# Kernel tuning notes

Hardware: AMD Instinct MI355X
Metric: run time of the kernel (lower is better)

## Reference

```python
import jax, jax.numpy as jnp
import numpy as np

N_NODES = 50000
N_EDGES = 800000
IN_FEATS = 128
H_FEATS = 128
OUT_FEATS = 64


def _mean_agg(h, src, dst, n_nodes):
    # mean over in-neighbors: sum h[src] into dst, divide by in-degree (0 for isolated nodes)
    summed = jax.ops.segment_sum(h[src], dst, num_segments=n_nodes)  # [N, d]
    deg = jax.ops.segment_sum(jnp.ones((src.shape[0],), h.dtype), dst, num_segments=n_nodes)
    return summed / jnp.maximum(deg, 1.0)[:, None]


def setup_inputs() -> dict:
    key = jax.random.key(0)
    ks = jax.random.split(key, 10)
    s = 0.05
    return {
        "inputs": jax.random.normal(ks[0], (N_NODES, IN_FEATS), jnp.float32),
        "fc_W": jax.random.normal(ks[1], (H_FEATS, IN_FEATS), jnp.float32) * s,
        "fc_b": jax.random.normal(ks[2], (H_FEATS,), jnp.float32) * s,
        "W": jax.random.normal(ks[3], (3, H_FEATS, H_FEATS), jnp.float32) * s,
        "b": jax.random.normal(ks[4], (3, H_FEATS), jnp.float32) * s,
        "W_last": jax.random.normal(ks[5], (OUT_FEATS, H_FEATS), jnp.float32) * s,
        "b_last": jax.random.normal(ks[6], (OUT_FEATS,), jnp.float32) * s,
        "eps": jnp.zeros((4,), jnp.float32),
        "src": jax.random.randint(ks[7], (N_EDGES,), 0, N_NODES, jnp.int32),
        "dst": jax.random.randint(ks[8], (N_EDGES,), 0, N_NODES, jnp.int32),
    }


def reference(inputs, fc_W, fc_b, W, b, W_last, b_last, eps, src, dst):
    n = inputs.shape[0]
    # input SLP
    h = jax.nn.relu(inputs @ fc_W.T + fc_b)
    # 3 hidden GIN layers: relu(Linear((1+eps)*h + mean_agg(h)))  (dropout = eval identity)
    for i in range(3):
        agg = _mean_agg(h, src, dst, n)
        h = jax.nn.relu(((1.0 + eps[i]) * h + agg) @ W[i].T + b[i])
    # last GIN layer (no ReLU)
    agg = _mean_agg(h, src, dst, n)
    h = ((1.0 + eps[3]) * h + agg) @ W_last.T + b_last
    return h
```

## Files before the change

### kernel.cpp

```cpp
#include <hip/hip_runtime.h>

#define N_NODES 50000
#define N_EDGES 800000
#define NBUCK 196
#define CAP 4608
#define CSTRIDE 16
#define EPB 4096
#define NSTRIPE ((N_EDGES + EPB - 1) / EPB)
#define GEMMB 782
#define WSPLB 224

typedef __attribute__((ext_vector_type(8))) short short8;
typedef __attribute__((ext_vector_type(4))) float float4v;

__device__ inline unsigned short f2bf(float f) {
    unsigned u = __float_as_uint(f);
    unsigned r = u + 0x7fff + ((u >> 16) & 1);
    return (unsigned short)(r >> 16);
}
__device__ inline float bf2f(unsigned short h) {
    return __uint_as_float(((unsigned)h) << 16);
}

__device__ __forceinline__ void split8(const float* __restrict__ p, short8& hi8, short8& lo8) {
    float4 f0 = *(const float4*)p;
    float4 f1 = *(const float4*)(p + 4);
    float fv[8] = {f0.x, f0.y, f0.z, f0.w, f1.x, f1.y, f1.z, f1.w};
#pragma unroll
    for (int j = 0; j < 8; j++) {
        unsigned short hh = f2bf(fv[j]);
        hi8[j] = (short)hh;
        lo8[j] = (short)f2bf(fv[j] - bf2f(hh));
    }
}


__device__ __forceinline__ void gather_sum(const unsigned short* __restrict__ bf,
                                           const int* __restrict__ esrc, int beg, int end,
                                           int eg, int fo, float a0[8]) {
    float a1[8], a2[8], a3[8];
#pragma unroll
    for (int j = 0; j < 8; j++) { a0[j] = 0.f; a1[j] = 0.f; a2[j] = 0.f; a3[j] = 0.f; }
    int e = beg;
    for (; e + 15 < end; e += 16) {
        int s0 = esrc[e + eg];
        int s1 = esrc[e + 4 + eg];
        int s2 = esrc[e + 8 + eg];
        int s3 = esrc[e + 12 + eg];
        short8 v0 = *(const short8*)(bf + (size_t)s0 * 128 + fo * 8);
        short8 v1 = *(const short8*)(bf + (size_t)s1 * 128 + fo * 8);
        short8 v2 = *(const short8*)(bf + (size_t)s2 * 128 + fo * 8);
        short8 v3 = *(const short8*)(bf + (size_t)s3 * 128 + fo * 8);
#pragma unroll
        for (int j = 0; j < 8; j++) a0[j] += bf2f((unsigned short)v0[j]);
#pragma unroll
        for (int j = 0; j < 8; j++) a1[j] += bf2f((unsigned short)v1[j]);
#pragma unroll
        for (int j = 0; j < 8; j++) a2[j] += bf2f((unsigned short)v2[j]);
#pragma unroll
        for (int j = 0; j < 8; j++) a3[j] += bf2f((unsigned short)v3[j]);
    }
    if (e + 7 < end) {
        int s0 = esrc[e + eg];
        int s1 = esrc[e + 4 + eg];
        short8 v0 = *(const short8*)(bf + (size_t)s0 * 128 + fo * 8);
        short8 v1 = *(const short8*)(bf + (size_t)s1 * 128 + fo * 8);
#pragma unroll
        for (int j = 0; j < 8; j++) a0[j] += bf2f((unsigned short)v0[j]);
#pragma unroll
        for (int j = 0; j < 8; j++) a1[j] += bf2f((unsigned short)v1[j]);
        e += 8;
    }
    if (e + 3 < end) {
        int s = esrc[e + eg];
        short8 v = *(const short8*)(bf + (size_t)s * 128 + fo * 8);
#pragma unroll
        for (int j = 0; j < 8; j++) a2[j] += bf2f((unsigned short)v[j]);
        e += 4;
    }
    int rem = end - e;
    if (eg < rem) {
        int s = esrc[e + eg];
        short8 v = *(const short8*)(bf + (size_t)s * 128 + fo * 8);
#pragma unroll
        for (int j = 0; j < 8; j++) a3[j] += bf2f((unsigned short)v[j]);
    }
#pragma unroll
    for (int j = 0; j < 8; j++) {
        float s = (a0[j] + a1[j]) + (a2[j] + a3[j]);
        s += __shfl_xor(s, 16);
        s += __shfl_xor(s, 32);
        a0[j] = s;
    }
}


__device__ __forceinline__ void slp_gemm(int bx, const float* __restrict__ X,
                                         const float* __restrict__ fcW,
                                         const float* __restrict__ fcb, float* __restrict__ h,
                                         unsigned short* __restrict__ hbf) {
    int wave = threadIdx.x >> 6;
    int lane = threadIdx.x & 63;
    int m = lane & 15;
    int quad = lane >> 4;
    int r0 = bx * 64 + wave * 16;
    int rowA = r0 + m;
    if (rowA >= N_NODES) rowA = N_NODES - 1;

    short8 ahi[4], alo[4];
    const float* arow = X + (size_t)rowA * 128 + quad * 8;
#pragma unroll
    for (int kc = 0; kc < 4; kc++) split8(arow + kc * 32, ahi[kc], alo[kc]);

#pragma unroll
    for (int nt = 0; nt < 8; nt++) {
        int n = nt * 16 + m;
        const float* brow = fcW + (size_t)n * 128 + quad * 8;
        float4v acc = {0.f, 0.f, 0.f, 0.f};
#pragma unroll
        for (int kc = 0; kc < 4; kc++) {
            short8 bh, bl;
            split8(brow + kc * 32, bh, bl);
            acc = __builtin_amdgcn_mfma_f32_16x16x32_bf16(ahi[kc], bh, acc, 0, 0, 0);
            acc = __builtin_amdgcn_mfma_f32_16x16x32_bf16(alo[kc], bh, acc, 0, 0, 0);
            acc = __builtin_amdgcn_mfma_f32_16x16x32_bf16(ahi[kc], bl, acc, 0, 0, 0);
        }
        float bv = fcb[n];
#pragma unroll
        for (int i = 0; i < 4; i++) {
            int r = r0 + quad * 4 + i;
            if (r < N_NODES) {
                float v = fmaxf(acc[i] + bv, 0.f);
                h[(size_t)r * 128 + n] = v;
                hbf[(size_t)r * 128 + n] = f2bf(v);
            }
        }
    }
}


__global__ void __launch_bounds__(256) fused_binA_gemm(
    const int* __restrict__ src, const int* __restrict__ dst, int* __restrict__ cursor,
    int* __restrict__ packed, const float* __restrict__ X, const float* __restrict__ fcW,
    const float* __restrict__ fcb, const float* __restrict__ W, const float* __restrict__ Wl,
    unsigned short* __restrict__ whi, unsigned short* __restrict__ wlo, float* __restrict__ h,
    unsigned short* __restrict__ hbf) {
    int bx = blockIdx.x;
    if (bx < NSTRIPE) {
        __shared__ int lcount[256];
        __shared__ int lbase[256];
        int t = threadIdx.x;
        lcount[t] = 0;
        __syncthreads();
        int base = bx * EPB + t;
#pragma unroll 4
        for (int k = 0; k < EPB / 256; k++) {
            int i = base + k * 256;
            if (i < N_EDGES) atomicAdd(&lcount[((unsigned)dst[i]) >> 8], 1);
        }
        __syncthreads();
        if (t < NBUCK) {
            lbase[t] = t * CAP + atomicAdd(&cursor[t * CSTRIDE], lcount[t]);
            lcount[t] = 0;
        }
        __syncthreads();
#pragma unroll 4
        for (int k = 0; k < EPB / 256; k++) {
            int i = base + k * 256;
            if (i < N_EDGES) {
                int d = dst[i];
                int wb = ((unsigned)d) >> 8;
                int p = lbase[wb] + atomicAdd(&lcount[wb], 1);
                if (p < (wb + 1) * CAP)
                    packed[p] = ((d & 255) << 16) | src[i];
            }
        }
    } else if (bx < NSTRIPE + GEMMB) {
        slp_gemm(bx - NSTRIPE, X, fcW, fcb, h, hbf);
    } else {
        int i = (bx - NSTRIPE - GEMMB) * 256 + threadIdx.x + 16384;
        if (i < 73728) {
            float v = (i < 65536) ? W[i - 16384] : Wl[i - 65536];
            unsigned short hh = f2bf(v);
            whi[i] = hh;
            wlo[i] = f2bf(v - bf2f(hh));
        }
    }
}


__global__ void __launch_bounds__(256) binB_kernel(const int* __restrict__ packed,
                                                   const int* __restrict__ cursor,
                                                   int* __restrict__ row_ptr,
                                                   int* __restrict__ esrc) {
    __shared__ int sm[256];
    __shared__ int cntS[256];
    __shared__ int curs[256];
    int b = blockIdx.x;
    int t = threadIdx.x;
    int cnt = (t < NBUCK) ? cursor[t * CSTRIDE] : 0;
    cntS[t] = cnt;
    sm[t] = cnt;
    __syncthreads();
    for (int o = 1; o < 256; o <<= 1) {
        int x = sm[t];
        int a = (t >= o) ? sm[t - o] : 0;
        __syncthreads();
        sm[t] = x + a;
        __syncthreads();
    }
    int w0 = sm[b] - cntS[b];
    int mycnt = cntS[b];
    int total = sm[NBUCK - 1];
    __syncthreads();
    if (b == NBUCK - 1 && t == 0) row_ptr[N_NODES] = total;
    int e0r = b * CAP, e1r = b * CAP + mycnt;
    curs[t] = 0;
    __syncthreads();
    for (int i = e0r + t; i < e1r; i += 256) atomicAdd(&curs[((unsigned)packed[i]) >> 16], 1);
    __syncthreads();
    int v = curs[t];
    sm[t] = v;
    __syncthreads();
    for (int o = 1; o < 256; o <<= 1) {
        int x = sm[t];
        int a = (t >= o) ? sm[t - o] : 0;
        __syncthreads();
        sm[t] = x + a;
        __syncthreads();
    }
    int excl = sm[t] - v;
    curs[t] = excl;
    int node = b * 256 + t;
    if (node < N_NODES) row_ptr[node] = w0 + excl;
    __syncthreads();
    for (int i = e0r + t; i < e1r; i += 256) {
        unsigned w = (unsigned)packed[i];
        int p = atomicAdd(&curs[w >> 16], 1);
        esrc[w0 + p] = (int)(w & 0xFFFFu);
    }
}


template <bool LAST>
__global__ void __launch_bounds__(512) layer_fused(
    float* __restrict__ hio, const unsigned short* __restrict__ bfin,
    unsigned short* __restrict__ bfout, const int* __restrict__ row_ptr,
    const int* __restrict__ esrc, const float* __restrict__ eps, int layer,
    const unsigned short* __restrict__ Whi, const unsigned short* __restrict__ Wlo,
    const float* __restrict__ bias, const unsigned short* __restrict__ Lhi,
    const unsigned short* __restrict__ Llo, float* __restrict__ g,
    unsigned short* __restrict__ gbf) {
    __shared__ unsigned lds_hi[16 * 64];
    __shared__ unsigned lds_lo[16 * 64];
    int tid = threadIdx.x;
    int wv = tid >> 6;
    int lane = tid & 63;
    int eg = lane >> 4;
    int fo = lane & 15;
    int nb = blockIdx.x * 16;
    float ep = 1.0f + eps[layer];

#pragma unroll
    for (int half = 0; half < 2; half++) {
        int r = wv + half * 8;
        int node = nb + r;
        int beg = __builtin_amdgcn_readfirstlane(row_ptr[node]);
        int end = __builtin_amdgcn_readfirstlane(row_ptr[node + 1]);
        float a0[8];
        gather_sum(bfin, esrc, beg, end, eg, fo, a0);
        if (eg == 0) {
            int d = end - beg;
            float inv = (d > 0) ? 1.0f / (float)d : 0.0f;
            const float* hr = hio + (size_t)node * 128 + fo * 8;
            float4 h0 = *(const float4*)hr;
            float4 h1 = *(const float4*)(hr + 4);
            float hv[8] = {h0.x, h0.y, h0.z, h0.w, h1.x, h1.y, h1.z, h1.w};
            unsigned hip[4], lop[4];
#pragma unroll
            for (int jj = 0; jj < 4; jj++) {
                float ux = ep * hv[2 * jj] + a0[2 * jj] * inv;
                float uy = ep * hv[2 * jj + 1] + a0[2 * jj + 1] * inv;
                unsigned short uh0 = f2bf(ux), uh1 = f2bf(uy);
                hip[jj] = (unsigned)uh0 | ((unsigned)uh1 << 16);
                lop[jj] = (unsigned)f2bf(ux - bf2f(uh0)) | ((unsigned)f2bf(uy - bf2f(uh1)) << 16);
            }
            int grp = fo ^ (r & 7);
            *(uint4*)&lds_hi[r * 64 + grp * 4] = make_uint4(hip[0], hip[1], hip[2], hip[3]);
            *(uint4*)&lds_lo[r * 64 + grp * 4] = make_uint4(lop[0], lop[1], lop[2], lop[3]);
        }
    }
    __syncthreads();

    int m = lane & 15;
    int quad = lane >> 4;
    short8 ahi[4], alo[4];
#pragma unroll
    for (int kc = 0; kc < 4; kc++) {
        int grp = (quad + kc * 4) ^ (m & 7);
        ahi[kc] = *(const short8*)&lds_hi[m * 64 + grp * 4];
        alo[kc] = *(const short8*)&lds_lo[m * 64 + grp * 4];
    }
    int n = wv * 16 + m;
    const unsigned short* bhp = Whi + (size_t)n * 128 + quad * 8;
    const unsigned short* blp = Wlo + (size_t)n * 128 + quad * 8;
    float4v acc = {0.f, 0.f, 0.f, 0.f};
#pragma unroll
    for (int kc = 0; kc < 4; kc++) {
        short8 bh = *(const short8*)(bhp + kc * 32);
        short8 bl = *(const short8*)(blp + kc * 32);
        acc = __builtin_amdgcn_mfma_f32_16x16x32_bf16(ahi[kc], bh, acc, 0, 0, 0);
        acc = __builtin_amdgcn_mfma_f32_16x16x32_bf16(alo[kc], bh, acc, 0, 0, 0);
        acc = __builtin_amdgcn_mfma_f32_16x16x32_bf16(ahi[kc], bl, acc, 0, 0, 0);
    }
    float bv = bias[n];

    if (!LAST) {
#pragma unroll
        for (int i = 0; i < 4; i++) {
            int rg = nb + quad * 4 + i;
            float v = fmaxf(acc[i] + bv, 0.f);
            hio[(size_t)rg * 128 + n] = v;
            bfout[(size_t)rg * 128 + n] = f2bf(v);
        }
    } else {
        __syncthreads();
        unsigned short* lh = (unsigned short*)lds_hi;
        unsigned short* ll = (unsigned short*)lds_lo;
#pragma unroll
        for (int i = 0; i < 4; i++) {
            int rl = quad * 4 + i;
            float v = fmaxf(acc[i] + bv, 0.f);
            unsigned short vh = f2bf(v);
            unsigned short vl = f2bf(v - bf2f(vh));
            int gidx = (n >> 3) ^ (rl & 7);
            int us = rl * 128 + gidx * 8 + (n & 7);
            lh[us] = vh;
            ll[us] = vl;
        }
        __syncthreads();
        if (wv < 4) {
            short8 a2h[4], a2l[4];
#pragma unroll
            for (int kc = 0; kc < 4; kc++) {
                int grp = (quad + kc * 4) ^ (m & 7);
                a2h[kc] = *(const short8*)&lds_hi[m * 64 + grp * 4];
                a2l[kc] = *(const short8*)&lds_lo[m * 64 + grp * 4];
            }
            int n2 = wv * 16 + m;
            const unsigned short* lhp = Lhi + (size_t)n2 * 128 + quad * 8;
            const unsigned short* llp = Llo + (size_t)n2 * 128 + quad * 8;
            float4v a2 = {0.f, 0.f, 0.f, 0.f};
#pragma unroll
            for (int kc = 0; kc < 4; kc++) {
                short8 bh = *(const short8*)(lhp + kc * 32);
                short8 bl = *(const short8*)(llp + kc * 32);
                a2 = __builtin_amdgcn_mfma_f32_16x16x32_bf16(a2h[kc], bh, a2, 0, 0, 0);
                a2 = __builtin_amdgcn_mfma_f32_16x16x32_bf16(a2l[kc], bh, a2, 0, 0, 0);
                a2 = __builtin_amdgcn_mfma_f32_16x16x32_bf16(a2h[kc], bl, a2, 0, 0, 0);
            }
#pragma unroll
            for (int i = 0; i < 4; i++) {
                int rg = nb + quad * 4 + i;
                float v = a2[i];
                g[(size_t)rg * 64 + n2] = v;
                gbf[(size_t)rg * 64 + n2] = f2bf(v);
            }
        }
    }
}


__global__ void __launch_bounds__(256) agg64_out(
    const float* __restrict__ g, const unsigned short* __restrict__ gbf,
    const int* __restrict__ row_ptr, const int* __restrict__ esrc,
    const float* __restrict__ eps, const float* __restrict__ bl, float* __restrict__ out) {
    int gtid = blockIdx.x * 256 + threadIdx.x;
    int node = gtid >> 6;
    if (node >= N_NODES) return;
    int lane = threadIdx.x & 63;
    node = __builtin_amdgcn_readfirstlane(node);
    int beg = __builtin_amdgcn_readfirstlane(row_ptr[node]);
    int end = __builtin_amdgcn_readfirstlane(row_ptr[node + 1]);
    int eg = lane >> 3;
    int fo = lane & 7;

    float a0[8] = {0.f, 0.f, 0.f, 0.f, 0.f, 0.f, 0.f, 0.f};
    float a1[8] = {0.f, 0.f, 0.f, 0.f, 0.f, 0.f, 0.f, 0.f};
    float a2[8] = {0.f, 0.f, 0.f, 0.f, 0.f, 0.f, 0.f, 0.f};
    float a3[8] = {0.f, 0.f, 0.f, 0.f, 0.f, 0.f, 0.f, 0.f};
    int e = beg;
    for (; e + 31 < end; e += 32) {
        int s0 = esrc[e + eg];
        int s1 = esrc[e + 8 + eg];
        int s2 = esrc[e + 16 + eg];
        int s3 = esrc[e + 24 + eg];
        short8 v0 = *(const short8*)(gbf + (size_t)s0 * 64 + fo * 8);
        short8 v1 = *(const short8*)(gbf + (size_t)s1 * 64 + fo * 8);
        short8 v2 = *(const short8*)(gbf + (size_t)s2 * 64 + fo * 8);
        short8 v3 = *(const short8*)(gbf + (size_t)s3 * 64 + fo * 8);
#pragma unroll
        for (int j = 0; j < 8; j++) a0[j] += bf2f((unsigned short)v0[j]);
#pragma unroll
        for (int j = 0; j < 8; j++) a1[j] += bf2f((unsigned short)v1[j]);
#pragma unroll
        for (int j = 0; j < 8; j++) a2[j] += bf2f((unsigned short)v2[j]);
#pragma unroll
        for (int j = 0; j < 8; j++) a3[j] += bf2f((unsigned short)v3[j]);
    }
    if (e + 15 < end) {
        int s0 = esrc[e + eg];
        int s1 = esrc[e + 8 + eg];
        short8 v0 = *(const short8*)(gbf + (size_t)s0 * 64 + fo * 8);
        short8 v1 = *(const short8*)(gbf + (size_t)s1 * 64 + fo * 8);
#pragma unroll
        for (int j = 0; j < 8; j++) a0[j] += bf2f((unsigned short)v0[j]);
#pragma unroll
        for (int j = 0; j < 8; j++) a1[j] += bf2f((unsigned short)v1[j]);
        e += 16;
    }
    if (e + 7 < end) {
        int s = esrc[e + eg];
        short8 v = *(const short8*)(gbf + (size_t)s * 64 + fo * 8);
#pragma unroll
        for (int j = 0; j < 8; j++) a2[j] += bf2f((unsigned short)v[j]);
        e += 8;
    }
    int rem = end - e;
    if (eg < rem) {
        int s = esrc[e + eg];
        short8 v = *(const short8*)(gbf + (size_t)s * 64 + fo * 8);
#pragma unroll
        for (int j = 0; j < 8; j++) a3[j] += bf2f((unsigned short)v[j]);
    }
#pragma unroll
    for (int j = 0; j < 8; j++) {
        float s = (a0[j] + a1[j]) + (a2[j] + a3[j]);
        s += __shfl_xor(s, 8);
        s += __shfl_xor(s, 16);
        s += __shfl_xor(s, 32);
        a0[j] = s;
    }
    if (eg == 0) {
        int d = end - beg;
        float inv = (d > 0) ? 1.0f / (float)d : 0.0f;
        float ep = 1.0f + eps[3];
        const float* gr = g + (size_t)node * 64 + fo * 8;
        float4 g0 = *(const float4*)gr;
        float4 g1 = *(const float4*)(gr + 4);
        const float* blr = bl + fo * 8;
        float4 b0 = *(const float4*)blr;
        float4 b1 = *(const float4*)(blr + 4);
        float4 r0, r1;
        r0.x = ep * g0.x + a0[0] * inv + b0.x;
        r0.y = ep * g0.y + a0[1] * inv + b0.y;
        r0.z = ep * g0.z + a0[2] * inv + b0.z;
        r0.w = ep * g0.w + a0[3] * inv + b0.w;
        r1.x = ep * g1.x + a0[4] * inv + b1.x;
        r1.y = ep * g1.y + a0[5] * inv + b1.y;
        r1.z = ep * g1.z + a0[6] * inv + b1.z;
        r1.w = ep * g1.w + a0[7] * inv + b1.w;
        float* op = out + (size_t)node * 64 + fo * 8;
        *(float4*)op = r0;
        *(float4*)(op + 4) = r1;
    }
}


extern "C" void kernel_launch(void* const* d_in, const int* in_sizes, int n_in,
                              void* d_out, int out_size, void* d_ws, size_t ws_size,
                              hipStream_t stream) {
    const float* X   = (const float*)d_in[0];
    const float* fcW = (const float*)d_in[1];
    const float* fcb = (const float*)d_in[2];
    const float* W   = (const float*)d_in[3];
    const float* b   = (const float*)d_in[4];
    const float* Wl  = (const float*)d_in[5];
    const float* bl  = (const float*)d_in[6];
    const float* eps = (const float*)d_in[7];
    const int* src   = (const int*)d_in[8];
    const int* dst   = (const int*)d_in[9];
    float* out = (float*)d_out;

    float* h = (float*)d_ws;
    unsigned short* bfA = (unsigned short*)(h + (size_t)N_NODES * 128);
    unsigned short* bfB = bfA + (size_t)N_NODES * 128;
    unsigned short* whi = bfB + (size_t)N_NODES * 128;
    unsigned short* wlo = whi + 73728;
    int* cursor  = (int*)(wlo + 73728);
    int* row_ptr = cursor + NBUCK * CSTRIDE;
    int* packed  = row_ptr + N_NODES + 1;
    int* esrc    = packed + NBUCK * CAP;
    unsigned short* gbf = (unsigned short*)(esrc + N_EDGES);
    float* g = (float*)bfB;

    const int agg_blocks = (N_NODES * 64 + 255) / 256;
    const int layer_blocks = N_NODES / 16;

    hipMemsetAsync(cursor, 0, NBUCK * CSTRIDE * sizeof(int), stream);
    fused_binA_gemm<<<NSTRIPE + GEMMB + WSPLB, 256, 0, stream>>>(
        src, dst, cursor, packed, X, fcW, fcb, W, Wl, whi, wlo, h, bfA);
    binB_kernel<<<NBUCK, 196 > 0 ? 256 : 256, 0, stream>>>(packed, cursor, row_ptr, esrc);

    layer_fused<false><<<layer_blocks, 512, 0, stream>>>(
        h, bfA, bfB, row_ptr, esrc, eps, 0, whi + 16384, wlo + 16384, b,
        nullptr, nullptr, nullptr, nullptr);
    layer_fused<false><<<layer_blocks, 512, 0, stream>>>(
        h, bfB, bfA, row_ptr, esrc, eps, 1, whi + 32768, wlo + 32768, b + 128,
        nullptr, nullptr, nullptr, nullptr);
    layer_fused<true><<<layer_blocks, 512, 0, stream>>>(
        h, bfA, nullptr, row_ptr, esrc, eps, 2, whi + 49152, wlo + 49152, b + 256,
        whi + 65536, wlo + 65536, g, gbf);

    agg64_out<<<agg_blocks, 256, 0, stream>>>(g, gbf, row_ptr, esrc, eps, bl, out);
}
```

Measured before the change: 387.6 us.

## Halve layer block to 8 nodes with 256 threads, two N-tiles per wave

The fused GIN layer kernel now handles 8 nodes per block with 4 waves instead of 16 nodes with 8 waves. Each wave computes two 16-column output tiles, so the full 128 columns are still covered. The MFMA tiles stay 16 rows tall, so half of each tile is padding that gets computed and then discarded: only quads 0-1 store results. The aim is finer-grained scheduling, so the irregular-degree gather balances better across CUs. The cost is twice the MFMA and weight-load work per node.

Measured after the change: 412.7 us. 6.5% more time.

```diff
diff --git a/kernel.cpp b/kernel.cpp
--- a/kernel.cpp
+++ b/kernel.cpp
@@ -243,7 +243,7 @@
 
 
 template <bool LAST>
-__global__ void __launch_bounds__(512) layer_fused(
+__global__ void __launch_bounds__(256) layer_fused(
     float* __restrict__ hio, const unsigned short* __restrict__ bfin,
     unsigned short* __restrict__ bfout, const int* __restrict__ row_ptr,
     const int* __restrict__ esrc, const float* __restrict__ eps, int layer,
@@ -258,12 +258,12 @@
     int lane = tid & 63;
     int eg = lane >> 4;
     int fo = lane & 15;
-    int nb = blockIdx.x * 16;
+    int nb = blockIdx.x * 8;
     float ep = 1.0f + eps[layer];
 
 #pragma unroll
     for (int half = 0; half < 2; half++) {
-        int r = wv + half * 8;
+        int r = wv + half * 4;
         int node = nb + r;
         int beg = __builtin_amdgcn_readfirstlane(row_ptr[node]);
         int end = __builtin_amdgcn_readfirstlane(row_ptr[node + 1]);
@@ -301,64 +301,82 @@
         ahi[kc] = *(const short8*)&lds_hi[m * 64 + grp * 4];
         alo[kc] = *(const short8*)&lds_lo[m * 64 + grp * 4];
     }
-    int n = wv * 16 + m;
-    const unsigned short* bhp = Whi + (size_t)n * 128 + quad * 8;
-    const unsigned short* blp = Wlo + (size_t)n * 128 + quad * 8;
-    float4v acc = {0.f, 0.f, 0.f, 0.f};
-#pragma unroll
-    for (int kc = 0; kc < 4; kc++) {
-        short8 bh = *(const short8*)(bhp + kc * 32);
-        short8 bl = *(const short8*)(blp + kc * 32);
-        acc = __builtin_amdgcn_mfma_f32_16x16x32_bf16(ahi[kc], bh, acc, 0, 0, 0);
-        acc = __builtin_amdgcn_mfma_f32_16x16x32_bf16(alo[kc], bh, acc, 0, 0, 0);
-        acc = __builtin_amdgcn_mfma_f32_16x16x32_bf16(ahi[kc], bl, acc, 0, 0, 0);
-    }
-    float bv = bias[n];
+    float4v acc[2];
+    float bv[2];
+#pragma unroll
+    for (int t2 = 0; t2 < 2; t2++) {
+        int n = (wv * 2 + t2) * 16 + m;
+        const unsigned short* bhp = Whi + (size_t)n * 128 + quad * 8;
+        const unsigned short* blp = Wlo + (size_t)n * 128 + quad * 8;
+        float4v a = {0.f, 0.f, 0.f, 0.f};
+#pragma unroll
+        for (int kc = 0; kc < 4; kc++) {
+            short8 bh = *(const short8*)(bhp + kc * 32);
+            short8 bl = *(const short8*)(blp + kc * 32);
+            a = __builtin_amdgcn_mfma_f32_16x16x32_bf16(ahi[kc], bh, a, 0, 0, 0);
+            a = __builtin_amdgcn_mfma_f32_16x16x32_bf16(alo[kc], bh, a, 0, 0, 0);
+            a = __builtin_amdgcn_mfma_f32_16x16x32_bf16(ahi[kc], bl, a, 0, 0, 0);
+        }
+        acc[t2] = a;
+        bv[t2] = bias[n];
+    }
 
     if (!LAST) {
 #pragma unroll
-        for (int i = 0; i < 4; i++) {
-            int rg = nb + quad * 4 + i;
-            float v = fmaxf(acc[i] + bv, 0.f);
-            hio[(size_t)rg * 128 + n] = v;
-            bfout[(size_t)rg * 128 + n] = f2bf(v);
+        for (int t2 = 0; t2 < 2; t2++) {
+            int n = (wv * 2 + t2) * 16 + m;
+            if (quad < 2) {
+#pragma unroll
+                for (int i = 0; i < 4; i++) {
+                    int rg = nb + quad * 4 + i;
+                    float v = fmaxf(acc[t2][i] + bv[t2], 0.f);
+                    hio[(size_t)rg * 128 + n] = v;
+                    bfout[(size_t)rg * 128 + n] = f2bf(v);
+                }
+            }
         }
     } else {
         __syncthreads();
         unsigned short* lh = (unsigned short*)lds_hi;
         unsigned short* ll = (unsigned short*)lds_lo;
 #pragma unroll
-        for (int i = 0; i < 4; i++) {
-            int rl = quad * 4 + i;
-            float v = fmaxf(acc[i] + bv, 0.f);
-            unsigned short vh = f2bf(v);
-            unsigned short vl = f2bf(v - bf2f(vh));
-            int gidx = (n >> 3) ^ (rl & 7);
-            int us = rl * 128 + gidx * 8 + (n & 7);
-            lh[us] = vh;
-            ll[us] = vl;
-        }
-        __syncthreads();
-        if (wv < 4) {
-            short8 a2h[4], a2l[4];
-#pragma unroll
-            for (int kc = 0; kc < 4; kc++) {
-                int grp = (quad + kc * 4) ^ (m & 7);
-                a2h[kc] = *(const short8*)&lds_hi[m * 64 + grp * 4];
-                a2l[kc] = *(const short8*)&lds_lo[m * 64 + grp * 4];
+        for (int t2 = 0; t2 < 2; t2++) {
+            int n = (wv * 2 + t2) * 16 + m;
+            if (quad < 2) {
+#pragma unroll
+                for (int i = 0; i < 4; i++) {
+                    int rl = quad * 4 + i;
+                    float v = fmaxf(acc[t2][i] + bv[t2], 0.f);
+                    unsigned short vh = f2bf(v);
+                    unsigned short vl = f2bf(v - bf2f(vh));
+                    int gidx = (n >> 3) ^ rl;
+                    int us = rl * 128 + gidx * 8 + (n & 7);
+                    lh[us] = vh;
+                    ll[us] = vl;
+                }
             }
-            int n2 = wv * 16 + m;
-            const unsigned short* lhp = Lhi + (size_t)n2 * 128 + quad * 8;
-            const unsigned short* llp = Llo + (size_t)n2 * 128 + quad * 8;
-            float4v a2 = {0.f, 0.f, 0.f, 0.f};
-#pragma unroll
-            for (int kc = 0; kc < 4; kc++) {
-                short8 bh = *(const short8*)(lhp + kc * 32);
-                short8 bl = *(const short8*)(llp + kc * 32);
-                a2 = __builtin_amdgcn_mfma_f32_16x16x32_bf16(a2h[kc], bh, a2, 0, 0, 0);
-                a2 = __builtin_amdgcn_mfma_f32_16x16x32_bf16(a2l[kc], bh, a2, 0, 0, 0);
-                a2 = __builtin_amdgcn_mfma_f32_16x16x32_bf16(a2h[kc], bl, a2, 0, 0, 0);
-            }
+        }
+        __syncthreads();
+        short8 a2h[4], a2l[4];
+#pragma unroll
+        for (int kc = 0; kc < 4; kc++) {
+            int grp = (quad + kc * 4) ^ (m & 7);
+            a2h[kc] = *(const short8*)&lds_hi[m * 64 + grp * 4];
+            a2l[kc] = *(const short8*)&lds_lo[m * 64 + grp * 4];
+        }
+        int n2 = wv * 16 + m;
+        const unsigned short* lhp = Lhi + (size_t)n2 * 128 + quad * 8;
+        const unsigned short* llp = Llo + (size_t)n2 * 128 + quad * 8;
+        float4v a2 = {0.f, 0.f, 0.f, 0.f};
+#pragma unroll
+        for (int kc = 0; kc < 4; kc++) {
+            short8 bh = *(const short8*)(lhp + kc * 32);
+            short8 bl = *(const short8*)(llp + kc * 32);
+            a2 = __builtin_amdgcn_mfma_f32_16x16x32_bf16(a2h[kc], bh, a2, 0, 0, 0);
+            a2 = __builtin_amdgcn_mfma_f32_16x16x32_bf16(a2l[kc], bh, a2, 0, 0, 0);
+            a2 = __builtin_amdgcn_mfma_f32_16x16x32_bf16(a2h[kc], bl, a2, 0, 0, 0);
+        }
+        if (quad < 2) {
 #pragma unroll
             for (int i = 0; i < 4; i++) {
                 int rg = nb + quad * 4 + i;
@@ -495,20 +513,20 @@
     float* g = (float*)bfB;
 
     const int agg_blocks = (N_NODES * 64 + 255) / 256;
-    const int layer_blocks = N_NODES / 16;
+    const int layer_blocks = N_NODES / 8;
 
     hipMemsetAsync(cursor, 0, NBUCK * CSTRIDE * sizeof(int), stream);
     fused_binA_gemm<<<NSTRIPE + GEMMB + WSPLB, 256, 0, stream>>>(
         src, dst, cursor, packed, X, fcW, fcb, W, Wl, whi, wlo, h, bfA);
-    binB_kernel<<<NBUCK, 196 > 0 ? 256 : 256, 0, stream>>>(packed, cursor, row_ptr, esrc);
-
-    layer_fused<false><<<layer_blocks, 512, 0, stream>>>(
+    binB_kernel<<<NBUCK, 256, 0, stream>>>(packed, cursor, row_ptr, esrc);
+
+    layer_fused<false><<<layer_blocks, 256, 0, stream>>>(
         h, bfA, bfB, row_ptr, esrc, eps, 0, whi + 16384, wlo + 16384, b,
         nullptr, nullptr, nullptr, nullptr);
-    layer_fused<false><<<layer_blocks, 512, 0, stream>>>(
+    layer_fused<false><<<layer_blocks, 256, 0, stream>>>(
         h, bfB, bfA, row_ptr, esrc, eps, 1, whi + 32768, wlo + 32768, b + 128,
         nullptr, nullptr, nullptr, nullptr);
-    layer_fused<true><<<layer_blocks, 512, 0, stream>>>(
+    layer_fused<true><<<layer_blocks, 256, 0, stream>>>(
         h, bfA, nullptr, row_ptr, esrc, eps, 2, whi + 49152, wlo + 49152, b + 256,
         whi + 65536, wlo + 65536, g, gbf);
 
```

## Merge all GIN stages into one persistent cooperative kernel with grid syncs

Applied to the files above, without the earlier changes.

Replaces the sequence of six kernel launches (binning, bucket sort, three fused layers, final aggregation) with a single persistent cooperative kernel that loops over work units and separates phases with grid-wide syncs. Block size goes to 512 and the SLP tile to 128 rows, and the edge binning now holds dst values in registers across its two passes. The aim is to remove launch gaps and tail effects between kernels. The cost is a fixed grid sized from occupancy, shared LDS reused across phases, extra block barriers, dropped __restrict__ qualifiers, and the expense of grid syncs.

Result: slower. 879.8 us (+127.0%).

```diff
diff --git a/kernel.cpp b/kernel.cpp
--- a/kernel.cpp
+++ b/kernel.cpp
@@ -1,4 +1,7 @@
 #include <hip/hip_runtime.h>
+#include <hip/hip_cooperative_groups.h>
+
+namespace cg = cooperative_groups;
 
 #define N_NODES 50000
 #define N_EDGES 800000
@@ -7,8 +10,11 @@
 #define CSTRIDE 16
 #define EPB 4096
 #define NSTRIPE ((N_EDGES + EPB - 1) / EPB)
-#define GEMMB 782
-#define WSPLB 224
+#define BLK 512
+#define SLPB ((N_NODES + 127) / 128)
+#define WSPLU ((73728 - 16384) / BLK)
+#define NTILE (N_NODES / 16)
+#define MAXGRID 1024
 
 typedef __attribute__((ext_vector_type(8))) short short8;
 typedef __attribute__((ext_vector_type(4))) float float4v;
@@ -22,7 +28,7 @@
     return __uint_as_float(((unsigned)h) << 16);
 }
 
-__device__ __forceinline__ void split8(const float* __restrict__ p, short8& hi8, short8& lo8) {
+__device__ __forceinline__ void split8(const float* p, short8& hi8, short8& lo8) {
     float4 f0 = *(const float4*)p;
     float4 f1 = *(const float4*)(p + 4);
     float fv[8] = {f0.x, f0.y, f0.z, f0.w, f1.x, f1.y, f1.z, f1.w};
@@ -35,9 +41,8 @@
 }
 
 
-__device__ __forceinline__ void gather_sum(const unsigned short* __restrict__ bf,
-                                           const int* __restrict__ esrc, int beg, int end,
-                                           int eg, int fo, float a0[8]) {
+__device__ __forceinline__ void gather_sum(const unsigned short* bf, const int* esrc,
+                                           int beg, int end, int eg, int fo, float a0[8]) {
     float a1[8], a2[8], a3[8];
 #pragma unroll
     for (int j = 0; j < 8; j++) { a0[j] = 0.f; a1[j] = 0.f; a2[j] = 0.f; a3[j] = 0.f; }
@@ -95,15 +100,45 @@
 }
 
 
-__device__ __forceinline__ void slp_gemm(int bx, const float* __restrict__ X,
-                                         const float* __restrict__ fcW,
-                                         const float* __restrict__ fcb, float* __restrict__ h,
-                                         unsigned short* __restrict__ hbf) {
+__device__ void binA_stripe(int sb, const int* src, const int* dst, int* cursor,
+                            int* packed, int* lcount, int* lbase) {
+    int t = threadIdx.x;
+    if (t < 256) lcount[t] = 0;
+    __syncthreads();
+    int base = sb * EPB + t;
+    int d[EPB / BLK];
+#pragma unroll
+    for (int k = 0; k < EPB / BLK; k++) {
+        int i = base + k * BLK;
+        d[k] = (i < N_EDGES) ? dst[i] : -1;
+        if (d[k] >= 0) atomicAdd(&lcount[((unsigned)d[k]) >> 8], 1);
+    }
+    __syncthreads();
+    if (t < NBUCK) {
+        lbase[t] = t * CAP + atomicAdd(&cursor[t * CSTRIDE], lcount[t]);
+        lcount[t] = 0;
+    }
+    __syncthreads();
+#pragma unroll
+    for (int k = 0; k < EPB / BLK; k++) {
+        if (d[k] >= 0) {
+            int i = base + k * BLK;
+            int wb = ((unsigned)d[k]) >> 8;
+            int p = lbase[wb] + atomicAdd(&lcount[wb], 1);
+            if (p < (wb + 1) * CAP) packed[p] = ((d[k] & 255) << 16) | src[i];
+        }
+    }
+    __syncthreads();
+}
+
+
+__device__ void slp_tile(int tile, const float* X, const float* fcW, const float* fcb,
+                         float* h, unsigned short* hbf) {
     int wave = threadIdx.x >> 6;
     int lane = threadIdx.x & 63;
     int m = lane & 15;
     int quad = lane >> 4;
-    int r0 = bx * 64 + wave * 16;
+    int r0 = tile * 128 + wave * 16;
     int rowA = r0 + m;
     if (rowA >= N_NODES) rowA = N_NODES - 1;
 
@@ -139,126 +174,70 @@
 }
 
 
-__global__ void __launch_bounds__(256) fused_binA_gemm(
-    const int* __restrict__ src, const int* __restrict__ dst, int* __restrict__ cursor,
-    int* __restrict__ packed, const float* __restrict__ X, const float* __restrict__ fcW,
-    const float* __restrict__ fcb, const float* __restrict__ W, const float* __restrict__ Wl,
-    unsigned short* __restrict__ whi, unsigned short* __restrict__ wlo, float* __restrict__ h,
-    unsigned short* __restrict__ hbf) {
-    int bx = blockIdx.x;
-    if (bx < NSTRIPE) {
-        __shared__ int lcount[256];
-        __shared__ int lbase[256];
-        int t = threadIdx.x;
-        lcount[t] = 0;
-        __syncthreads();
-        int base = bx * EPB + t;
-#pragma unroll 4
-        for (int k = 0; k < EPB / 256; k++) {
-            int i = base + k * 256;
-            if (i < N_EDGES) atomicAdd(&lcount[((unsigned)dst[i]) >> 8], 1);
-        }
-        __syncthreads();
-        if (t < NBUCK) {
-            lbase[t] = t * CAP + atomicAdd(&cursor[t * CSTRIDE], lcount[t]);
-            lcount[t] = 0;
-        }
-        __syncthreads();
-#pragma unroll 4
-        for (int k = 0; k < EPB / 256; k++) {
-            int i = base + k * 256;
-            if (i < N_EDGES) {
-                int d = dst[i];
-                int wb = ((unsigned)d) >> 8;
-                int p = lbase[wb] + atomicAdd(&lcount[wb], 1);
-                if (p < (wb + 1) * CAP)
-                    packed[p] = ((d & 255) << 16) | src[i];
-            }
-        }
-    } else if (bx < NSTRIPE + GEMMB) {
-        slp_gemm(bx - NSTRIPE, X, fcW, fcb, h, hbf);
-    } else {
-        int i = (bx - NSTRIPE - GEMMB) * 256 + threadIdx.x + 16384;
-        if (i < 73728) {
-            float v = (i < 65536) ? W[i - 16384] : Wl[i - 65536];
-            unsigned short hh = f2bf(v);
-            whi[i] = hh;
-            wlo[i] = f2bf(v - bf2f(hh));
-        }
-    }
-}
-
-
-__global__ void __launch_bounds__(256) binB_kernel(const int* __restrict__ packed,
-                                                   const int* __restrict__ cursor,
-                                                   int* __restrict__ row_ptr,
-                                                   int* __restrict__ esrc) {
-    __shared__ int sm[256];
-    __shared__ int cntS[256];
-    __shared__ int curs[256];
-    int b = blockIdx.x;
+__device__ void binB_bucket(int b, const int* packed, const int* cursor, int* row_ptr,
+                            int* esrc, int* sm, int* cntS, int* curs) {
     int t = threadIdx.x;
-    int cnt = (t < NBUCK) ? cursor[t * CSTRIDE] : 0;
-    cntS[t] = cnt;
-    sm[t] = cnt;
+    bool act = t < 256;
+    int cnt = (act && t < NBUCK) ? cursor[t * CSTRIDE] : 0;
+    if (act) { cntS[t] = cnt; sm[t] = cnt; }
     __syncthreads();
     for (int o = 1; o < 256; o <<= 1) {
-        int x = sm[t];
-        int a = (t >= o) ? sm[t - o] : 0;
-        __syncthreads();
-        sm[t] = x + a;
+        int x = act ? sm[t] : 0;
+        int a = (act && t >= o) ? sm[t - o] : 0;
+        __syncthreads();
+        if (act) sm[t] = x + a;
         __syncthreads();
     }
     int w0 = sm[b] - cntS[b];
     int mycnt = cntS[b];
-    int total = sm[NBUCK - 1];
-    __syncthreads();
-    if (b == NBUCK - 1 && t == 0) row_ptr[N_NODES] = total;
+    if (b == NBUCK - 1 && t == 0) row_ptr[N_NODES] = sm[NBUCK - 1];
+    __syncthreads();
     int e0r = b * CAP, e1r = b * CAP + mycnt;
-    curs[t] = 0;
-    __syncthreads();
-    for (int i = e0r + t; i < e1r; i += 256) atomicAdd(&curs[((unsigned)packed[i]) >> 16], 1);
-    __syncthreads();
-    int v = curs[t];
-    sm[t] = v;
+    if (act) curs[t] = 0;
+    __syncthreads();
+    for (int i = e0r + t; i < e1r; i += BLK) atomicAdd(&curs[((unsigned)packed[i]) >> 16], 1);
+    __syncthreads();
+    int v = act ? curs[t] : 0;
+    __syncthreads();
+    if (act) sm[t] = v;
     __syncthreads();
     for (int o = 1; o < 256; o <<= 1) {
-        int x = sm[t];
-        int a = (t >= o) ? sm[t - o] : 0;
-        __syncthreads();
-        sm[t] = x + a;
-        __syncthreads();
-    }
-    int excl = sm[t] - v;
-    curs[t] = excl;
-    int node = b * 256 + t;
-    if (node < N_NODES) row_ptr[node] = w0 + excl;
-    __syncthreads();
-    for (int i = e0r + t; i < e1r; i += 256) {
+        int x = act ? sm[t] : 0;
+        int a = (act && t >= o) ? sm[t - o] : 0;
+        __syncthreads();
+        if (act) sm[t] = x + a;
+        __syncthreads();
+    }
+    if (act) {
+        int excl = sm[t] - v;
+        curs[t] = excl;
+        int node = b * 256 + t;
+        if (node < N_NODES) row_ptr[node] = w0 + excl;
+    }
+    __syncthreads();
+    for (int i = e0r + t; i < e1r; i += BLK) {
         unsigned w = (unsigned)packed[i];
         int p = atomicAdd(&curs[w >> 16], 1);
         esrc[w0 + p] = (int)(w & 0xFFFFu);
     }
+    __syncthreads();
 }
 
 
 template <bool LAST>
-__global__ void __launch_bounds__(512) layer_fused(
-    float* __restrict__ hio, const unsigned short* __restrict__ bfin,
-    unsigned short* __restrict__ bfout, const int* __restrict__ row_ptr,
-    const int* __restrict__ esrc, const float* __restrict__ eps, int layer,
-    const unsigned short* __restrict__ Whi, const unsigned short* __restrict__ Wlo,
-    const float* __restrict__ bias, const unsigned short* __restrict__ Lhi,
-    const unsigned short* __restrict__ Llo, float* __restrict__ g,
-    unsigned short* __restrict__ gbf) {
-    __shared__ unsigned lds_hi[16 * 64];
-    __shared__ unsigned lds_lo[16 * 64];
+__device__ void layer_tile(int tile, float* hio, const unsigned short* bfin,
+                           unsigned short* bfout, const int* row_ptr, const int* esrc,
+                           const float* eps, int layer, const unsigned short* Whi,
+                           const unsigned short* Wlo, const float* bias,
+                           const unsigned short* Lhi, const unsigned short* Llo,
+                           float* g, unsigned short* gbf, unsigned* lds_hi,
+                           unsigned* lds_lo) {
     int tid = threadIdx.x;
     int wv = tid >> 6;
     int lane = tid & 63;
     int eg = lane >> 4;
     int fo = lane & 15;
-    int nb = blockIdx.x * 16;
+    int nb = tile * 16;
     float ep = 1.0f + eps[layer];
 
 #pragma unroll
@@ -323,6 +302,7 @@
             hio[(size_t)rg * 128 + n] = v;
             bfout[(size_t)rg * 128 + n] = f2bf(v);
         }
+        __syncthreads();
     } else {
         __syncthreads();
         unsigned short* lh = (unsigned short*)lds_hi;
@@ -367,19 +347,15 @@
                 gbf[(size_t)rg * 64 + n2] = f2bf(v);
             }
         }
-    }
-}
-
-
-__global__ void __launch_bounds__(256) agg64_out(
-    const float* __restrict__ g, const unsigned short* __restrict__ gbf,
-    const int* __restrict__ row_ptr, const int* __restrict__ esrc,
-    const float* __restrict__ eps, const float* __restrict__ bl, float* __restrict__ out) {
-    int gtid = blockIdx.x * 256 + threadIdx.x;
-    int node = gtid >> 6;
-    if (node >= N_NODES) return;
+        __syncthreads();
+    }
+}
+
+
+__device__ void agg64_node(int node, const float* g, const unsigned short* gbf,
+                           const int* row_ptr, const int* esrc, const float* eps,
+                           const float* bl, float* out) {
     int lane = threadIdx.x & 63;
-    node = __builtin_amdgcn_readfirstlane(node);
     int beg = __builtin_amdgcn_readfirstlane(row_ptr[node]);
     int end = __builtin_amdgcn_readfirstlane(row_ptr[node + 1]);
     int eg = lane >> 3;
@@ -467,9 +443,64 @@
 }
 
 
+__global__ void __launch_bounds__(BLK, 8) gin_coop(
+    const int* src, const int* dst, int* cursor, int* packed, const float* X,
+    const float* fcW, const float* fcb, const float* W, const float* Wl, const float* b,
+    const float* bl, const float* eps, unsigned short* whi, unsigned short* wlo, float* h,
+    unsigned short* bfA, unsigned short* bfB, int* row_ptr, int* esrc, float* g,
+    unsigned short* gbf, float* out) {
+    cg::grid_group gg = cg::this_grid();
+    __shared__ unsigned smhi[16 * 64];
+    __shared__ unsigned smlo[16 * 64];
+    int G = gridDim.x;
+
+    for (int u = blockIdx.x; u < NSTRIPE + SLPB + WSPLU; u += G) {
+        if (u < NSTRIPE) {
+            binA_stripe(u, src, dst, cursor, packed, (int*)smhi, (int*)smlo);
+        } else if (u < NSTRIPE + SLPB) {
+            slp_tile(u - NSTRIPE, X, fcW, fcb, h, bfA);
+        } else {
+            int i = (u - NSTRIPE - SLPB) * BLK + threadIdx.x + 16384;
+            if (i < 73728) {
+                float v = (i < 65536) ? W[i - 16384] : Wl[i - 65536];
+                unsigned short hh = f2bf(v);
+                whi[i] = hh;
+                wlo[i] = f2bf(v - bf2f(hh));
+            }
+        }
+    }
+    gg.sync();
+
+    for (int u = blockIdx.x; u < NBUCK; u += G)
+        binB_bucket(u, packed, cursor, row_ptr, esrc, (int*)smhi, (int*)smhi + 256,
+                    (int*)smlo);
+    gg.sync();
+
+    for (int t = blockIdx.x; t < NTILE; t += G)
+        layer_tile<false>(t, h, bfA, bfB, row_ptr, esrc, eps, 0, whi + 16384, wlo + 16384,
+                          b, nullptr, nullptr, nullptr, nullptr, smhi, smlo);
+    gg.sync();
+    for (int t = blockIdx.x; t < NTILE; t += G)
+        layer_tile<false>(t, h, bfB, bfA, row_ptr, esrc, eps, 1, whi + 32768, wlo + 32768,
+                          b + 128, nullptr, nullptr, nullptr, nullptr, smhi, smlo);
+    gg.sync();
+    for (int t = blockIdx.x; t < NTILE; t += G)
+        layer_tile<true>(t, h, bfA, nullptr, row_ptr, esrc, eps, 2, whi + 49152,
+                         wlo + 49152, b + 256, whi + 65536, wlo + 65536, g, gbf, smhi,
+                         smlo);
+    gg.sync();
+
+    int gw = blockIdx.x * (BLK / 64) + (threadIdx.x >> 6);
+    for (int node = gw; node < N_NODES; node += G * (BLK / 64))
+        agg64_node(node, g, gbf, row_ptr, esrc, eps, bl, out);
+}
+
+
 extern "C" void kernel_launch(void* const* d_in, const int* in_sizes, int n_in,
                               void* d_out, int out_size, void* d_ws, size_t ws_size,
                               hipStream_t stream) {
+    const int* src   = (const int*)d_in[8];
+    const int* dst   = (const int*)d_in[9];
     const float* X   = (const float*)d_in[0];
     const float* fcW = (const float*)d_in[1];
     const float* fcb = (const float*)d_in[2];
@@ -478,8 +509,6 @@
     const float* Wl  = (const float*)d_in[5];
     const float* bl  = (const float*)d_in[6];
     const float* eps = (const float*)d_in[7];
-    const int* src   = (const int*)d_in[8];
-    const int* dst   = (const int*)d_in[9];
     float* out = (float*)d_out;
 
     float* h = (float*)d_ws;
@@ -494,23 +523,20 @@
     unsigned short* gbf = (unsigned short*)(esrc + N_EDGES);
     float* g = (float*)bfB;
 
-    const int agg_blocks = (N_NODES * 64 + 255) / 256;
-    const int layer_blocks = N_NODES / 16;
+    int maxb = 2;
+    if (hipOccupancyMaxActiveBlocksPerMultiprocessor(&maxb, gin_coop, BLK, 0) !=
+            hipSuccess ||
+        maxb < 1)
+        maxb = 2;
+    int grid = maxb * 256;
+    if (grid > MAXGRID) grid = MAXGRID;
 
     hipMemsetAsync(cursor, 0, NBUCK * CSTRIDE * sizeof(int), stream);
-    fused_binA_gemm<<<NSTRIPE + GEMMB + WSPLB, 256, 0, stream>>>(
-        src, dst, cursor, packed, X, fcW, fcb, W, Wl, whi, wlo, h, bfA);
-    binB_kernel<<<NBUCK, 196 > 0 ? 256 : 256, 0, stream>>>(packed, cursor, row_ptr, esrc);
-
-    layer_fused<false><<<layer_blocks, 512, 0, stream>>>(
-        h, bfA, bfB, row_ptr, esrc, eps, 0, whi + 16384, wlo + 16384, b,
-        nullptr, nullptr, nullptr, nullptr);
-    layer_fused<false><<<layer_blocks, 512, 0, stream>>>(
-        h, bfB, bfA, row_ptr, esrc, eps, 1, whi + 32768, wlo + 32768, b + 128,
-        nullptr, nullptr, nullptr, nullptr);
-    layer_fused<true><<<layer_blocks, 512, 0, stream>>>(
-        h, bfA, nullptr, row_ptr, esrc, eps, 2, whi + 49152, wlo + 49152, b + 256,
-        whi + 65536, wlo + 65536, g, gbf);
-
-    agg64_out<<<agg_blocks, 256, 0, stream>>>(g, gbf, row_ptr, esrc, eps, bl, out);
-}
+
+    void* args[] = {(void*)&src, (void*)&dst, (void*)&cursor, (void*)&packed, (void*)&X,
+                    (void*)&fcW, (void*)&fcb, (void*)&W,      (void*)&Wl,     (void*)&b,
+                    (void*)&bl,  (void*)&eps, (void*)&whi,    (void*)&wlo,    (void*)&h,
+                    (void*)&bfA, (void*)&bfB, (void*)&row_ptr, (void*)&esrc,  (void*)&g,
+                    (void*)&gbf, (void*)&out};
+    hipLaunchCooperativeKernel((void*)gin_coop, dim3(grid), dim3(BLK), args, 0, stream);
+}
```
